# Performance work log

Hardware: AMD Instinct MI355X
Metric: run time of the kernel (lower is better)

The kernel has to match this reference:

```python
import jax, jax.numpy as jnp
import numpy as np

D = 512      # feature dim d
N = 8192     # context length n
LMBD = 0.9   # eligibility trace decay


def _build_consts():
    two_d1 = 2 * D + 1
    # P: single nonzero entry at bottom-right
    P = np.zeros((two_d1, two_d1), dtype=np.float32)
    P[-1, -1] = 1.0
    # M: (n+1)x(n+1); top-left n x n block is lower-triangular lmbd^(row-col),
    # last row and last column are all zero (M[-1,-1] set to 0 in torch code)
    i = np.arange(N)
    diff = i[:, None] - i[None, :]
    Mnn = np.where(diff >= 0, LMBD ** np.maximum(diff, 0), 0.0).astype(np.float32)
    M = np.zeros((N + 1, N + 1), dtype=np.float32)
    M[:N, :N] = Mnn
    # Q: top-left 2d x 2d block = [[-I, I], [0, 0]]
    I = np.eye(D, dtype=np.float32)
    Q = np.zeros((two_d1, two_d1), dtype=np.float32)
    Q[:D, :D] = -I
    Q[:D, D:2 * D] = I
    return jnp.asarray(P), jnp.asarray(M), jnp.asarray(Q)


def setup_inputs() -> dict:
    key = jax.random.key(0)
    kz, = jax.random.split(key, 1)
    Z = jax.random.normal(kz, (2 * D + 1, N + 1), dtype=jnp.float32)
    alpha = jnp.ones((1,), dtype=jnp.float32)  # learned parameter
    P, M, Q = _build_consts()
    return {"Z": Z, "alpha": alpha, "P": P, "M": M, "Q": Q}


def reference(Z, alpha, P, M, Q):
    # Z: (2d+1, n+1). Matches torch: Z + alpha/n * P @ Z @ M @ Z.T @ Q @ Z
    n = Z.shape[1] - 1
    upd = ((((P @ Z) @ M) @ Z.T) @ Q) @ Z  # left-to-right like torch's @ chain
    return Z + (alpha[0] / n) * upd
```

## Files before the change

kernel.cpp:

```cpp
#include <hip/hip_runtime.h>

#define ND   512
#define NN   8192
#define NP1  8193

typedef float f4 __attribute__((ext_vector_type(4)));

#define NWB   512
#define NCPB  512
#define CTHR  131072u
#define HI_BEG   1048704u
#define LAST_BEG 2097408u
#define F4_END   2099456u
#define TAILF    8397824u

__device__ __forceinline__ int sw(int j) { return j + (j >> 5); }
#define ZSLEN 8448

__global__ __launch_bounds__(256) void kMain(const float* __restrict__ Z,
                                             float* __restrict__ w,
                                             float* __restrict__ out) {
    const int b = blockIdx.x;
    const int t = threadIdx.x;

    if (b < NWB) {
        __shared__ float zs[ZSLEN];
        __shared__ float es[256];
        __shared__ float red[4];
        const int c = b;
        const size_t base = (size_t)c * NP1;
        const int pre = (4 - (c & 3)) & 3;
        const int nq  = (NP1 - pre) >> 2;

        const f4* __restrict__ src = (const f4*)(Z + base + pre);
        f4* __restrict__ dst = (f4*)(out + base + pre);

        f4 xv[8];
#pragma unroll
        for (int m = 0; m < 8; ++m) {
            int i = t + 256 * m;
            xv[m] = (i < nq) ? src[i] : (f4){0.f, 0.f, 0.f, 0.f};
        }
#pragma unroll
        for (int m = 0; m < 8; ++m) {
            int i = t + 256 * m;
            if (i < nq) __builtin_nontemporal_store(xv[m], &dst[i]);
        }
#pragma unroll
        for (int m = 0; m < 8; ++m) {
            int i = t + 256 * m;
            if (i < nq) {
                int j = pre + 4 * i;
#pragma unroll
                for (int e = 0; e < 4; ++e)
                    if (j + e < NN) zs[sw(j + e)] = xv[m][e];
            }
        }
        if (t == 0) {
            for (int e = 0; e < pre; ++e) {
                float zv = Z[base + e];
                __builtin_nontemporal_store(zv, &out[base + e]);
                zs[sw(e)] = zv;
            }
            for (int j = pre + 4 * nq; j < NP1; ++j) {
                float zv = Z[base + j];
                __builtin_nontemporal_store(zv, &out[base + j]);
                if (j < NN) zs[sw(j)] = zv;
            }
        }
        __syncthreads();

        float r[32];
#pragma unroll
        for (int i = 0; i < 32; ++i) r[i] = zs[sw(32 * t + i)];

        const float L1 = 0.9f;
        float e = r[0];
#pragma unroll
        for (int i = 1; i < 32; ++i) e = fmaf(L1, e, r[i]);
        es[t] = e;
        __syncthreads();

        const float l2 = L1 * L1, l4v = l2 * l2, l8 = l4v * l4v;
        const float l16 = l8 * l8, lam32 = l16 * l16;
        float C = 0.f;
#pragma unroll
        for (int k = 7; k >= 1; --k) {
            float ek = (t - k >= 0) ? es[t - k] : 0.f;
            C = fmaf(lam32, C, ek);
        }

        float qv = C;
#pragma unroll
        for (int i = 0; i < 32; ++i) {
            qv = fmaf(L1, qv, r[i]);
            zs[sw(32 * t + i)] = qv;
        }
        __syncthreads();

        const f4* __restrict__ zrow4 = (const f4*)(Z + (size_t)(2 * ND) * NP1);
        float a0 = 0.f, a1 = 0.f, a2 = 0.f, a3 = 0.f;
#pragma unroll
        for (int m = 0; m < 8; ++m) {
            int i = t + 256 * m;
            f4 zv = zrow4[i];
            int j = 4 * i;
            a0 = fmaf(zv[0], zs[sw(j)],     a0);
            a1 = fmaf(zv[1], zs[sw(j + 1)], a1);
            a2 = fmaf(zv[2], zs[sw(j + 2)], a2);
            a3 = fmaf(zv[3], zs[sw(j + 3)], a3);
        }
        float acc = (a0 + a1) + (a2 + a3);

        for (int off = 32; off > 0; off >>= 1)
            acc += __shfl_down(acc, off, 64);
        if ((t & 63) == 0) red[t >> 6] = acc;
        __syncthreads();
        if (t == 0) w[c] = (red[0] + red[1]) + (red[2] + red[3]);
    } else {
        const f4* __restrict__ src = (const f4*)Z;
        f4* __restrict__ dst = (f4*)out;
        unsigned tid = (unsigned)(b - NWB) * 256u + (unsigned)t;
        unsigned i = HI_BEG + tid;
#pragma unroll
        for (int m = 0; m < 8; ++m) {
            f4 x = src[i];
            __builtin_nontemporal_store(x, &dst[i]);
            i += CTHR;
        }
        if (i < F4_END) {
            f4 x = src[i];
            if (i >= LAST_BEG) dst[i] = x;
            else __builtin_nontemporal_store(x, &dst[i]);
        }
        if (tid == 0u) out[TAILF] = Z[TAILF];
    }
}

__global__ __launch_bounds__(256) void kFin(const float* __restrict__ Z,
                                            const float* __restrict__ w,
                                            const float* __restrict__ alpha,
                                            float* __restrict__ out) {
    int j = blockIdx.x * 256 + threadIdx.x;
    if (j >= NP1) return;
    int c0 = blockIdx.y * 16;
    const size_t DS = (size_t)ND * NP1;
    float acc0 = 0.f, acc1 = 0.f;
#pragma unroll
    for (int cb = 0; cb < 16; cb += 4) {
        int c = c0 + cb;
        size_t base = (size_t)c * NP1 + (size_t)j;
        float lo0 = Z[base          ], lo1 = Z[base +     NP1];
        float lo2 = Z[base + 2 * NP1], lo3 = Z[base + 3 * NP1];
        float hi0 = Z[base + DS          ], hi1 = Z[base + DS +     NP1];
        float hi2 = Z[base + DS + 2 * NP1], hi3 = Z[base + DS + 3 * NP1];
        acc0 = fmaf(w[c],     hi0 - lo0, acc0);
        acc1 = fmaf(w[c + 1], hi1 - lo1, acc1);
        acc0 = fmaf(w[c + 2], hi2 - lo2, acc0);
        acc1 = fmaf(w[c + 3], hi3 - lo3, acc1);
    }
    float s = alpha[0] * (1.0f / (float)NN);
    atomicAdd(&out[(size_t)(2 * ND) * NP1 + j], s * (acc0 + acc1));
}

extern "C" void kernel_launch(void* const* d_in, const int* in_sizes, int n_in,
                              void* d_out, int out_size, void* d_ws, size_t ws_size,
                              hipStream_t stream) {
    const float* Z     = (const float*)d_in[0];
    const float* alpha = (const float*)d_in[1];
    float* out = (float*)d_out;

    float* w = (float*)d_ws;

    kMain<<<NWB + NCPB, 256, 0, stream>>>(Z, w, out);
    kFin<<<dim3(33, 32), 256, 0, stream>>>(Z, w, alpha, out);
}
```

Before: 22.14 us.

## Fuse high-half copy of Z into the update kernel's reads

The bulk copy of Z's upper rows (rows 512..1024) to the output moves from dedicated copy blocks in the first kernel into the second kernel, which already loads those values to compute the update, so they are written with nontemporal stores from registers. The first kernel now only copies the final row (the atomicAdd target) before the second kernel runs. This removes a duplicate read of about 16 MB of Z, at the cost of making the second kernel store-heavy and serialising that copy after the w computation instead of overlapping it.

After: 23.11 us. 1.04x slower.

```diff
diff --git a/kernel.cpp b/kernel.cpp
--- a/kernel.cpp
+++ b/kernel.cpp
@@ -7,19 +7,13 @@
 typedef float f4 __attribute__((ext_vector_type(4)));
 
 #define NWB   512
-#define NCPB  512
-#define CTHR  131072u
-#define HI_BEG   1048704u
-#define LAST_BEG 2097408u
-#define F4_END   2099456u
-#define TAILF    8397824u
 
 __device__ __forceinline__ int sw(int j) { return j + (j >> 5); }
 #define ZSLEN 8448
 
-__global__ __launch_bounds__(256) void kMain(const float* __restrict__ Z,
-                                             float* __restrict__ w,
-                                             float* __restrict__ out) {
+__global__ __launch_bounds__(256) void kW(const float* __restrict__ Z,
+                                          float* __restrict__ w,
+                                          float* __restrict__ out) {
     const int b = blockIdx.x;
     const int t = threadIdx.x;
 
@@ -118,29 +112,19 @@
         __syncthreads();
         if (t == 0) w[c] = (red[0] + red[1]) + (red[2] + red[3]);
     } else {
-        const f4* __restrict__ src = (const f4*)Z;
-        f4* __restrict__ dst = (f4*)out;
-        unsigned tid = (unsigned)(b - NWB) * 256u + (unsigned)t;
-        unsigned i = HI_BEG + tid;
-#pragma unroll
-        for (int m = 0; m < 8; ++m) {
-            f4 x = src[i];
-            __builtin_nontemporal_store(x, &dst[i]);
-            i += CTHR;
-        }
-        if (i < F4_END) {
-            f4 x = src[i];
-            if (i >= LAST_BEG) dst[i] = x;
-            else __builtin_nontemporal_store(x, &dst[i]);
-        }
-        if (tid == 0u) out[TAILF] = Z[TAILF];
+        const size_t ZROW = (size_t)(2 * ND) * NP1;
+        const f4* __restrict__ src = (const f4*)(Z + ZROW);
+        f4* __restrict__ dst = (f4*)(out + ZROW);
+        int i = (b - NWB) * 256 + t;
+        dst[i] = src[i];
+        if (b == NWB && t == 0) out[ZROW + NN] = Z[ZROW + NN];
     }
 }
 
-__global__ __launch_bounds__(256) void kFin(const float* __restrict__ Z,
-                                            const float* __restrict__ w,
-                                            const float* __restrict__ alpha,
-                                            float* __restrict__ out) {
+__global__ __launch_bounds__(256) void kU(const float* __restrict__ Z,
+                                          const float* __restrict__ w,
+                                          const float* __restrict__ alpha,
+                                          float* __restrict__ out) {
     int j = blockIdx.x * 256 + threadIdx.x;
     if (j >= NP1) return;
     int c0 = blockIdx.y * 16;
@@ -154,6 +138,10 @@
         float lo2 = Z[base + 2 * NP1], lo3 = Z[base + 3 * NP1];
         float hi0 = Z[base + DS          ], hi1 = Z[base + DS +     NP1];
         float hi2 = Z[base + DS + 2 * NP1], hi3 = Z[base + DS + 3 * NP1];
+        __builtin_nontemporal_store(hi0, &out[base + DS          ]);
+        __builtin_nontemporal_store(hi1, &out[base + DS +     NP1]);
+        __builtin_nontemporal_store(hi2, &out[base + DS + 2 * NP1]);
+        __builtin_nontemporal_store(hi3, &out[base + DS + 3 * NP1]);
         acc0 = fmaf(w[c],     hi0 - lo0, acc0);
         acc1 = fmaf(w[c + 1], hi1 - lo1, acc1);
         acc0 = fmaf(w[c + 2], hi2 - lo2, acc0);
@@ -172,6 +160,6 @@
 
     float* w = (float*)d_ws;
 
-    kMain<<<NWB + NCPB, 256, 0, stream>>>(Z, w, out);
-    kFin<<<dim3(33, 32), 256, 0, stream>>>(Z, w, alpha, out);
+    kW<<<NWB + 8, 256, 0, stream>>>(Z, w, out);
+    kU<<<dim3(33, 32), 256, 0, stream>>>(Z, w, alpha, out);
 }
```
